# Optimization experiments

Measured on AMD Instinct MI355X. Metric: run time of the kernel, lower is better.

The kernel has to match this reference:

```python
import jax, jax.numpy as jnp
import numpy as np

HIDDEN = 2048
B, T, K = 64, 512, 49  # K = 7x7 spatial grid

def setup_inputs() -> dict:
    key = jax.random.key(0)
    ks = jax.random.split(key, 7)
    def xavier(k, shape):
        fan_in, fan_out = shape[1], shape[0]
        bound = float(np.sqrt(6.0 / (fan_in + fan_out)))
        return jax.random.uniform(k, shape, jnp.float32, -bound, bound)
    return {
        "V": jax.random.normal(ks[0], (B, K, HIDDEN), jnp.float32),
        "h_t": jax.random.normal(ks[1], (B, T, HIDDEN), jnp.float32),
        "sent_t": jax.random.normal(ks[2], (B, T, HIDDEN), jnp.float32),
        "Wv": xavier(ks[3], (K, HIDDEN)),
        "Wg": xavier(ks[4], (K, HIDDEN)),
        "Ws": xavier(ks[5], (K, HIDDEN)),
        "Wh": xavier(ks[6], (1, K)),
    }

def reference(V, h_t, sent_t, Wv, Wg, Ws, Wh):
    # Dropout is identity (eval mode / deterministic reference).
    wh = Wh[0]                                    # [K]
    pv = jnp.einsum('bkd,jd->bkj', V, Wv)         # [B,K,K]
    pg = jnp.einsum('btd,jd->btj', h_t, Wg)       # [B,T,K]
    content_v = pv[:, None, :, :] + pg[:, :, None, :]   # [B,T,K,K]
    z_t = jnp.tanh(content_v) @ wh                # [B,T,K]
    alpha_t = jax.nn.softmax(z_t, axis=-1)        # spatial attention
    c_t = jnp.einsum('btk,bkd->btd', alpha_t, V)  # [B,T,HIDDEN]
    content_s = jnp.einsum('btd,jd->btj', sent_t, Ws) + pg  # [B,T,K]
    z_ext = jnp.tanh(content_s) @ wh              # [B,T]
    extend = jnp.concatenate([z_t, z_ext[..., None]], axis=-1)  # [B,T,K+1]
    alpha_hat = jax.nn.softmax(extend, axis=-1)
    beta_t = alpha_hat[:, :, -1:]                 # sentinel gate [B,T,1]
    c_hat_t = beta_t * sent_t + (1.0 - beta_t) * c_t
    return (c_hat_t, alpha_t, beta_t)
```

## Files before the change

### kernel.cpp

```cpp
#include <hip/hip_runtime.h>

#define HIDDEN 2048
#define NB 64
#define NT 512
#define NK 49

typedef __attribute__((ext_vector_type(4))) float f32x4;
typedef __attribute__((ext_vector_type(8))) short short8;

__device__ __forceinline__ unsigned cvtpk_bf16(float a, float b) {
    unsigned r;
    asm("v_cvt_pk_bf16_f32 %0, %1, %2" : "=v"(r) : "v"(a), "v"(b));
    return r;
}

__device__ __forceinline__ unsigned short f2bf(float x) {
    union { float f; unsigned u; } v; v.f = x;
    unsigned r = v.u + 0x7FFF + ((v.u >> 16) & 1);
    return (unsigned short)(r >> 16);
}

__global__ __launch_bounds__(256) void convert_w(
    const float* __restrict__ Wg, const float* __restrict__ Ws,
    const float* __restrict__ Wv, unsigned short* __restrict__ Wf)
{
    int tau = blockIdx.x * 256 + threadIdx.x;
    int m   = tau >> 14;
    int rem = tau & 16383;
    int st  = rem >> 8;
    int c   = (rem >> 6) & 3;
    int l   = rem & 63;
    int col = c * 16 + (l & 15);
    int k0  = st * 32 + ((l >> 4) << 3);

    const float* W = (m == 0) ? Wg : (m == 1) ? Ws : Wv;
    unsigned short out[8];
    if (col < NK) {
        const float* p = W + (size_t)col * HIDDEN + k0;
        #pragma unroll
        for (int j = 0; j < 8; j++) out[j] = f2bf(p[j]);
    } else {
        #pragma unroll
        for (int j = 0; j < 8; j++) out[j] = 0;
    }
    unsigned short* dst = Wf + (size_t)tau * 8;
    #pragma unroll
    for (int j = 0; j < 8; j++) dst[j] = out[j];
}

__global__ __launch_bounds__(256) void gemm_mfma(
    const float* __restrict__ h, const float* __restrict__ s,
    const float* __restrict__ V, const unsigned short* __restrict__ Wf,
    float* __restrict__ pg, float* __restrict__ ps, float* __restrict__ pv)
{
    int w = threadIdx.x >> 6, lane = threadIdx.x & 63;
    int blk = blockIdx.x;

    const float* A; float* C; int rowBase; const unsigned short* wfm;
    if (blk < 512)       { A = h; C = pg; rowBase = blk * 64;          wfm = Wf; }
    else if (blk < 1024) { A = s; C = ps; rowBase = (blk - 512) * 64;  wfm = Wf + (size_t)16384 * 8; }
    else                 { A = V; C = pv; rowBase = (blk - 1024) * 64; wfm = Wf + (size_t)32768 * 8; }

    const float* ap = A + (size_t)(rowBase + w * 16 + (lane & 15)) * HIDDEN + ((lane >> 4) << 3);
    const short8* wfp = (const short8*)wfm;

    __shared__ short8 lb[2][1024];
    short8* lbp0 = &lb[0][0];
    short8* lbp1 = &lb[1][0];
    int q = w * 4;

    f32x4 acc0 = {0.f, 0.f, 0.f, 0.f};
    f32x4 acc1 = acc0, acc2 = acc0, acc3 = acc0;

    float4 a0_0, a0_1, a1_0, a1_1, a2_0, a2_1, a3_0, a3_1;
    short8 bs0, bs1, bs2, bs3;

#define LOADBS(ch) { \
    bs0 = wfp[(ch) * 1024 + (q + 0) * 64 + lane]; \
    bs1 = wfp[(ch) * 1024 + (q + 1) * 64 + lane]; \
    bs2 = wfp[(ch) * 1024 + (q + 2) * 64 + lane]; \
    bs3 = wfp[(ch) * 1024 + (q + 3) * 64 + lane]; }

#define WRITEBS(lbp) { \
    lbp[(q + 0) * 64 + lane] = bs0; \
    lbp[(q + 1) * 64 + lane] = bs1; \
    lbp[(q + 2) * 64 + lane] = bs2; \
    lbp[(q + 3) * 64 + lane] = bs3; }

#define LOADA2(A0, A1, gst) { \
    A0 = *(const float4*)(ap + (gst) * 32); \
    A1 = *(const float4*)(ap + (gst) * 32 + 4); }

#define STEP(lbp, sti, Aa, Ab, rgst, dorf) { \
    union { short8 v; unsigned u[4]; } a_; \
    a_.u[0] = cvtpk_bf16(Aa.x, Aa.y); \
    a_.u[1] = cvtpk_bf16(Aa.z, Aa.w); \
    a_.u[2] = cvtpk_bf16(Ab.x, Ab.y); \
    a_.u[3] = cvtpk_bf16(Ab.z, Ab.w); \
    short8 b0 = lbp[((sti) * 4 + 0) * 64 + lane]; \
    short8 b1 = lbp[((sti) * 4 + 1) * 64 + lane]; \
    short8 b2 = lbp[((sti) * 4 + 2) * 64 + lane]; \
    short8 b3 = lbp[((sti) * 4 + 3) * 64 + lane]; \
    if (dorf) { LOADA2(Aa, Ab, rgst) } \
    acc0 = __builtin_amdgcn_mfma_f32_16x16x32_bf16(a_.v, b0, acc0, 0, 0, 0); \
    acc1 = __builtin_amdgcn_mfma_f32_16x16x32_bf16(a_.v, b1, acc1, 0, 0, 0); \
    acc2 = __builtin_amdgcn_mfma_f32_16x16x32_bf16(a_.v, b2, acc2, 0, 0, 0); \
    acc3 = __builtin_amdgcn_mfma_f32_16x16x32_bf16(a_.v, b3, acc3, 0, 0, 0); }

    LOADBS(0)
    LOADA2(a0_0, a0_1, 0)
    LOADA2(a1_0, a1_1, 1)
    LOADA2(a2_0, a2_1, 2)
    LOADA2(a3_0, a3_1, 3)
    WRITEBS(lbp0)
    LOADBS(1)
    __syncthreads();

    #pragma unroll 1
    for (int ch = 0; ch < 16; ch++) {
        short8* cur = (ch & 1) ? lbp1 : lbp0;
        short8* nxt = (ch & 1) ? lbp0 : lbp1;
        if (ch < 15) { WRITEBS(nxt) }
        if (ch < 14) { LOADBS(ch + 2) }
        bool rf = ch < 15;
        int g = (ch + 1) * 4;
        STEP(cur, 0, a0_0, a0_1, g + 0, rf)
        STEP(cur, 1, a1_0, a1_1, g + 1, rf)
        STEP(cur, 2, a2_0, a2_1, g + 2, rf)
        STEP(cur, 3, a3_0, a3_1, g + 3, rf)
        __syncthreads();
    }

#undef LOADBS
#undef WRITEBS
#undef LOADA2
#undef STEP

    int colb  = lane & 15;
    int rquad = (lane >> 4) << 2;
    float* crow = C + (size_t)(rowBase + w * 16 + rquad) * NK + colb;
    #pragma unroll
    for (int r = 0; r < 4; r++) {
        crow[(size_t)r * NK + 0]  = acc0[r];
        crow[(size_t)r * NK + 16] = acc1[r];
        crow[(size_t)r * NK + 32] = acc2[r];
    }
    if (colb == 0) {
        #pragma unroll
        for (int r = 0; r < 4; r++) crow[(size_t)r * NK + 48] = acc3[r];
    }
}

__device__ __forceinline__ float ftanh(float x) {
    float e = __expf(2.f * x);
    return 1.f - 2.f * __builtin_amdgcn_rcpf(e + 1.f);
}

__global__ __launch_bounds__(256) void zab_kernel(
    const float* __restrict__ pg, const float* __restrict__ ps,
    const float* __restrict__ pv, const float* __restrict__ Wh,
    float* __restrict__ alpha, float* __restrict__ beta)
{
    int w = threadIdx.x >> 6, lane = threadIdx.x & 63;
    int row = blockIdx.x * 4 + w;
    int b = row >> 9;

    const float* pgrow = pg + (size_t)row * NK;
    const float* psrow = ps + (size_t)row * NK;

    float va = 0.f;
    if (lane < NK)
        va = ftanh(psrow[lane] + pgrow[lane]) * Wh[lane];
    float z_ext = va;
    #pragma unroll
    for (int off = 32; off; off >>= 1) z_ext += __shfl_xor(z_ext, off);

    float z = -1e30f;
    if (lane < NK) {
        const float* pvrow = pv + ((size_t)b * NK + lane) * NK;
        float acc = 0.f;
        for (int j = 0; j < NK; j++)
            acc = fmaf(ftanh(pvrow[j] + pgrow[j]), Wh[j], acc);
        z = acc;
    }

    float m = z;
    #pragma unroll
    for (int off = 32; off; off >>= 1) m = fmaxf(m, __shfl_xor(m, off));
    float p = (lane < NK) ? __expf(z - m) : 0.f;
    float ssum = p;
    #pragma unroll
    for (int off = 32; off; off >>= 1) ssum += __shfl_xor(ssum, off);
    float a = p * __builtin_amdgcn_rcpf(ssum);

    if (lane < NK)
        alpha[(size_t)row * NK + lane] = a;

    float me = fmaxf(m, z_ext);
    float se = ssum * __expf(m - me) + __expf(z_ext - me);
    float bet = __expf(z_ext - me) * __builtin_amdgcn_rcpf(se);
    if (lane == 0) beta[row] = bet;
}

__global__ __launch_bounds__(256) void chat_kernel(
    const float* __restrict__ V, const float* __restrict__ sent,
    const float* __restrict__ alpha, const float* __restrict__ beta,
    float* __restrict__ chat)
{
    int d0 = blockIdx.x * 128;
    int t0 = blockIdx.y * 32;
    int b  = blockIdx.z;

    __shared__ float alpha_s[NK][36];
    __shared__ float beta_s[32];

    int tid = threadIdx.x;

    const float* arow = alpha + ((size_t)b * NT + t0) * NK;
    for (int i = tid; i < 32 * NK; i += 256) {
        int t = i / NK, k = i - t * NK;
        alpha_s[k][t] = arow[i];
    }
    if (tid < 32) beta_s[tid] = beta[(size_t)b * NT + t0 + tid];
    __syncthreads();

    int tx = tid & 31;
    int ty = tid >> 5;

    const float* vp = V + (size_t)b * NK * HIDDEN + d0 + tx * 4;

    float4 acc[4];
    #pragma unroll
    for (int i = 0; i < 4; i++) acc[i] = make_float4(0.f, 0.f, 0.f, 0.f);

    #pragma unroll 7
    for (int k = 0; k < NK; k++) {
        float4 vv = *(const float4*)(vp + (size_t)k * HIDDEN);
        float4 a4 = *(const float4*)&alpha_s[k][ty * 4];
        acc[0].x = fmaf(a4.x, vv.x, acc[0].x);
        acc[0].y = fmaf(a4.x, vv.y, acc[0].y);
        acc[0].z = fmaf(a4.x, vv.z, acc[0].z);
        acc[0].w = fmaf(a4.x, vv.w, acc[0].w);
        acc[1].x = fmaf(a4.y, vv.x, acc[1].x);
        acc[1].y = fmaf(a4.y, vv.y, acc[1].y);
        acc[1].z = fmaf(a4.y, vv.z, acc[1].z);
        acc[1].w = fmaf(a4.y, vv.w, acc[1].w);
        acc[2].x = fmaf(a4.z, vv.x, acc[2].x);
        acc[2].y = fmaf(a4.z, vv.y, acc[2].y);
        acc[2].z = fmaf(a4.z, vv.z, acc[2].z);
        acc[2].w = fmaf(a4.z, vv.w, acc[2].w);
        acc[3].x = fmaf(a4.w, vv.x, acc[3].x);
        acc[3].y = fmaf(a4.w, vv.y, acc[3].y);
        acc[3].z = fmaf(a4.w, vv.z, acc[3].z);
        acc[3].w = fmaf(a4.w, vv.w, acc[3].w);
    }

    #pragma unroll
    for (int i = 0; i < 4; i++) {
        int t = ty * 4 + i;
        float bt = beta_s[t];
        const float* sp = sent + ((size_t)b * NT + t0 + t) * HIDDEN + d0 + tx * 4;
        float*       op = chat + ((size_t)b * NT + t0 + t) * HIDDEN + d0 + tx * 4;
        float4 sv = *(const float4*)sp;
        float4 o;
        o.x = fmaf(bt, sv.x, (1.f - bt) * acc[i].x);
        o.y = fmaf(bt, sv.y, (1.f - bt) * acc[i].y);
        o.z = fmaf(bt, sv.z, (1.f - bt) * acc[i].z);
        o.w = fmaf(bt, sv.w, (1.f - bt) * acc[i].w);
        *(float4*)op = o;
    }
}

extern "C" void kernel_launch(void* const* d_in, const int* in_sizes, int n_in,
                              void* d_out, int out_size, void* d_ws, size_t ws_size,
                              hipStream_t stream)
{
    const float* V    = (const float*)d_in[0];
    const float* h_t  = (const float*)d_in[1];
    const float* sent = (const float*)d_in[2];
    const float* Wv   = (const float*)d_in[3];
    const float* Wg   = (const float*)d_in[4];
    const float* Ws   = (const float*)d_in[5];
    const float* Wh   = (const float*)d_in[6];

    float* out   = (float*)d_out;
    float* chat  = out;
    float* alpha = out + (size_t)NB * NT * HIDDEN;
    float* beta  = alpha + (size_t)NB * NT * NK;

    float* ws = (float*)d_ws;
    float* pg = ws;
    float* ps = pg + (size_t)NB * NT * NK;
    float* pv = ps + (size_t)NB * NT * NK;
    unsigned short* Wf = (unsigned short*)(pv + (size_t)NB * NK * NK);

    convert_w<<<192, 256, 0, stream>>>(Wg, Ws, Wv, Wf);
    gemm_mfma<<<1073, 256, 0, stream>>>(h_t, sent, V, Wf, pg, ps, pv);
    zab_kernel<<<(NB * NT) / 4, 256, 0, stream>>>(pg, ps, pv, Wh, alpha, beta);
    chat_kernel<<<dim3(HIDDEN / 128, NT / 32, NB), 256, 0, stream>>>(V, sent, alpha, beta, chat);
}
```

Measured before the change: 351.7 us.

## Stream W tiles straight into LDS and double-buffer A chunks in registers

The projection GEMM now uses global_load_lds to copy the bf16 weight tiles directly from global memory into the LDS double buffer, instead of staging them through registers and writing them with ds_write. The fp32 A-operand loads move to inline-asm global_load_dwordx4 with two register sets (P and Q), so loads run a full chunk ahead of the MFMA work. The aim is to cut register pressure and LDS write instructions and to hide more HBM latency in this bandwidth-heavy GEMM. The inline-asm loads are invisible to the compiler's s_waitcnt tracking, so correctness depends on waits emitted for the DMA loads also covering them.

After: 354.6 us. Within noise of the previous version (+0.8%).

```diff
diff --git a/kernel.cpp b/kernel.cpp
--- a/kernel.cpp
+++ b/kernel.cpp
@@ -48,6 +48,38 @@
     for (int j = 0; j < 8; j++) dst[j] = out[j];
 }
 
+#define ALOADP(Ra, Rb, gst) { \
+    const float* _p = ap + (size_t)(gst) * 32; \
+    asm volatile("global_load_dwordx4 %0, %1, off" : "=v"(Ra) : "v"(_p)); \
+    asm volatile("global_load_dwordx4 %0, %1, off" : "=v"(Rb) : "v"(_p + 4)); }
+
+#define BDMA(srcch, buf) { \
+    const short8* _s = wfp + (size_t)(srcch) * 1024 + q * 64 + lane; \
+    __builtin_amdgcn_global_load_lds((const void*)(_s), \
+        (void*)&lb[buf][(q + 0) * 64], 16, 0, 0); \
+    __builtin_amdgcn_global_load_lds((const void*)(_s + 64), \
+        (void*)&lb[buf][(q + 1) * 64], 16, 0, 0); \
+    __builtin_amdgcn_global_load_lds((const void*)(_s + 128), \
+        (void*)&lb[buf][(q + 2) * 64], 16, 0, 0); \
+    __builtin_amdgcn_global_load_lds((const void*)(_s + 192), \
+        (void*)&lb[buf][(q + 3) * 64], 16, 0, 0); }
+
+#define STEP(Ra, Rb, lbc, sti, rgst, dorf) { \
+    union { short8 v; unsigned u[4]; } a_; \
+    a_.u[0] = cvtpk_bf16(Ra[0], Ra[1]); \
+    a_.u[1] = cvtpk_bf16(Ra[2], Ra[3]); \
+    a_.u[2] = cvtpk_bf16(Rb[0], Rb[1]); \
+    a_.u[3] = cvtpk_bf16(Rb[2], Rb[3]); \
+    short8 b0 = lbc[((sti) * 4 + 0) * 64 + lane]; \
+    short8 b1 = lbc[((sti) * 4 + 1) * 64 + lane]; \
+    short8 b2 = lbc[((sti) * 4 + 2) * 64 + lane]; \
+    short8 b3 = lbc[((sti) * 4 + 3) * 64 + lane]; \
+    if (dorf) { ALOADP(Ra, Rb, rgst) } \
+    acc0 = __builtin_amdgcn_mfma_f32_16x16x32_bf16(a_.v, b0, acc0, 0, 0, 0); \
+    acc1 = __builtin_amdgcn_mfma_f32_16x16x32_bf16(a_.v, b1, acc1, 0, 0, 0); \
+    acc2 = __builtin_amdgcn_mfma_f32_16x16x32_bf16(a_.v, b2, acc2, 0, 0, 0); \
+    acc3 = __builtin_amdgcn_mfma_f32_16x16x32_bf16(a_.v, b3, acc3, 0, 0, 0); }
+
 __global__ __launch_bounds__(256) void gemm_mfma(
     const float* __restrict__ h, const float* __restrict__ s,
     const float* __restrict__ V, const unsigned short* __restrict__ Wf,
@@ -65,76 +97,46 @@
     const short8* wfp = (const short8*)wfm;
 
     __shared__ short8 lb[2][1024];
-    short8* lbp0 = &lb[0][0];
-    short8* lbp1 = &lb[1][0];
     int q = w * 4;
 
     f32x4 acc0 = {0.f, 0.f, 0.f, 0.f};
     f32x4 acc1 = acc0, acc2 = acc0, acc3 = acc0;
 
-    float4 a0_0, a0_1, a1_0, a1_1, a2_0, a2_1, a3_0, a3_1;
-    short8 bs0, bs1, bs2, bs3;
-
-#define LOADBS(ch) { \
-    bs0 = wfp[(ch) * 1024 + (q + 0) * 64 + lane]; \
-    bs1 = wfp[(ch) * 1024 + (q + 1) * 64 + lane]; \
-    bs2 = wfp[(ch) * 1024 + (q + 2) * 64 + lane]; \
-    bs3 = wfp[(ch) * 1024 + (q + 3) * 64 + lane]; }
-
-#define WRITEBS(lbp) { \
-    lbp[(q + 0) * 64 + lane] = bs0; \
-    lbp[(q + 1) * 64 + lane] = bs1; \
-    lbp[(q + 2) * 64 + lane] = bs2; \
-    lbp[(q + 3) * 64 + lane] = bs3; }
-
-#define LOADA2(A0, A1, gst) { \
-    A0 = *(const float4*)(ap + (gst) * 32); \
-    A1 = *(const float4*)(ap + (gst) * 32 + 4); }
-
-#define STEP(lbp, sti, Aa, Ab, rgst, dorf) { \
-    union { short8 v; unsigned u[4]; } a_; \
-    a_.u[0] = cvtpk_bf16(Aa.x, Aa.y); \
-    a_.u[1] = cvtpk_bf16(Aa.z, Aa.w); \
-    a_.u[2] = cvtpk_bf16(Ab.x, Ab.y); \
-    a_.u[3] = cvtpk_bf16(Ab.z, Ab.w); \
-    short8 b0 = lbp[((sti) * 4 + 0) * 64 + lane]; \
-    short8 b1 = lbp[((sti) * 4 + 1) * 64 + lane]; \
-    short8 b2 = lbp[((sti) * 4 + 2) * 64 + lane]; \
-    short8 b3 = lbp[((sti) * 4 + 3) * 64 + lane]; \
-    if (dorf) { LOADA2(Aa, Ab, rgst) } \
-    acc0 = __builtin_amdgcn_mfma_f32_16x16x32_bf16(a_.v, b0, acc0, 0, 0, 0); \
-    acc1 = __builtin_amdgcn_mfma_f32_16x16x32_bf16(a_.v, b1, acc1, 0, 0, 0); \
-    acc2 = __builtin_amdgcn_mfma_f32_16x16x32_bf16(a_.v, b2, acc2, 0, 0, 0); \
-    acc3 = __builtin_amdgcn_mfma_f32_16x16x32_bf16(a_.v, b3, acc3, 0, 0, 0); }
-
-    LOADBS(0)
-    LOADA2(a0_0, a0_1, 0)
-    LOADA2(a1_0, a1_1, 1)
-    LOADA2(a2_0, a2_1, 2)
-    LOADA2(a3_0, a3_1, 3)
-    WRITEBS(lbp0)
-    LOADBS(1)
-    __syncthreads();
+    f32x4 P0, P1, P2, P3, P4, P5, P6, P7;
+    f32x4 Q0, Q1, Q2, Q3, Q4, Q5, Q6, Q7;
+
+    ALOADP(P0, P1, 0) ALOADP(P2, P3, 1) ALOADP(P4, P5, 2) ALOADP(P6, P7, 3)
+    BDMA(0, 0)
+    ALOADP(Q0, Q1, 4) ALOADP(Q2, Q3, 5) ALOADP(Q4, Q5, 6) ALOADP(Q6, Q7, 7)
 
     #pragma unroll 1
-    for (int ch = 0; ch < 16; ch++) {
-        short8* cur = (ch & 1) ? lbp1 : lbp0;
-        short8* nxt = (ch & 1) ? lbp0 : lbp1;
-        if (ch < 15) { WRITEBS(nxt) }
-        if (ch < 14) { LOADBS(ch + 2) }
-        bool rf = ch < 15;
-        int g = (ch + 1) * 4;
-        STEP(cur, 0, a0_0, a0_1, g + 0, rf)
-        STEP(cur, 1, a1_0, a1_1, g + 1, rf)
-        STEP(cur, 2, a2_0, a2_1, g + 2, rf)
-        STEP(cur, 3, a3_0, a3_1, g + 3, rf)
+    for (int tt = 0; tt < 8; tt++) {
+        int t0 = tt * 2, t1 = t0 + 1;
+
         __syncthreads();
-    }
-
-#undef LOADBS
-#undef WRITEBS
-#undef LOADA2
-#undef STEP
+        BDMA(t0 + 1, 1)
+        {
+            const short8* lbc = &lb[0][0];
+            bool rf = (t0 + 2) < 16;
+            int rg = (t0 + 2) * 4;
+            STEP(P0, P1, lbc, 0, rg + 0, rf)
+            STEP(P2, P3, lbc, 1, rg + 1, rf)
+            STEP(P4, P5, lbc, 2, rg + 2, rf)
+            STEP(P6, P7, lbc, 3, rg + 3, rf)
+        }
+
+        __syncthreads();
+        if (t1 + 1 < 16) { BDMA(t1 + 1, 0) }
+        {
+            const short8* lbc = &lb[1][0];
+            bool rf = (t1 + 2) < 16;
+            int rg = (t1 + 2) * 4;
+            STEP(Q0, Q1, lbc, 0, rg + 0, rf)
+            STEP(Q2, Q3, lbc, 1, rg + 1, rf)
+            STEP(Q4, Q5, lbc, 2, rg + 2, rf)
+            STEP(Q6, Q7, lbc, 3, rg + 3, rf)
+        }
+    }
 
     int colb  = lane & 15;
     int rquad = (lane >> 4) << 2;
```
